# Kernel tuning notes

Hardware: AMD Instinct MI355X
Metric: run time of the kernel (lower is better)

## Reference

```python
import jax, jax.numpy as jnp
import numpy as np

EPS = 1e-5
NUM_HEADS = 16


def layernorm(x, g, b):
    m = jnp.mean(x, axis=-1, keepdims=True)
    v = jnp.mean(jnp.square(x - m), axis=-1, keepdims=True)
    return (x - m) * jax.lax.rsqrt(v + EPS) * g + b


def setup_inputs() -> dict:
    key = jax.random.key(0)
    ks = jax.random.split(key, 8)
    B, S, E, F = 16, 512, 1024, 4096
    s_e = 1.0 / np.sqrt(E)
    s_f = 1.0 / np.sqrt(F)
    return {
        "input": jax.random.normal(ks[0], (B, S, E), jnp.float32),
        "ln1_g": jnp.ones((E,), jnp.float32),
        "ln1_b": jnp.zeros((E,), jnp.float32),
        "wq": jax.random.normal(ks[1], (E, E), jnp.float32) * s_e,
        "bq": jnp.zeros((E,), jnp.float32),
        "wk": jax.random.normal(ks[2], (E, E), jnp.float32) * s_e,
        "bk": jnp.zeros((E,), jnp.float32),
        "wv": jax.random.normal(ks[3], (E, E), jnp.float32) * s_e,
        "bv": jnp.zeros((E,), jnp.float32),
        "wo": jax.random.normal(ks[4], (E, E), jnp.float32) * s_e,
        "bo": jnp.zeros((E,), jnp.float32),
        "ln2_g": jnp.ones((E,), jnp.float32),
        "ln2_b": jnp.zeros((E,), jnp.float32),
        "w1": jax.random.normal(ks[5], (E, F), jnp.float32) * s_e,
        "b1": jnp.zeros((F,), jnp.float32),
        "w2": jax.random.normal(ks[6], (F, E), jnp.float32) * s_f,
        "b2": jnp.zeros((E,), jnp.float32),
    }


def attention(x, wq, bq, wk, bk, wv, bv, wo, bo):
    B, S, E = x.shape
    H = NUM_HEADS
    D = E // H
    q = (x @ wq + bq).reshape(B, S, H, D)
    k = (x @ wk + bk).reshape(B, S, H, D)
    v = (x @ wv + bv).reshape(B, S, H, D)
    scores = jnp.einsum("bqhd,bkhd->bhqk", q, k) * (1.0 / np.sqrt(D))
    attn = jax.nn.softmax(scores, axis=-1)
    out = jnp.einsum("bhqk,bkhd->bqhd", attn, v).reshape(B, S, E)
    return out @ wo + bo


def reference(input, ln1_g, ln1_b, wq, bq, wk, bk, wv, bv, wo, bo,
              ln2_g, ln2_b, w1, b1, w2, b2):
    # pre-LN attention + residual
    x = layernorm(input, ln1_g, ln1_b)
    x = attention(x, wq, bq, wk, bk, wv, bv, wo, bo)
    x = x + input
    # pre-LN MLP (GELU exact, matching nn.GELU default) + residual
    y = layernorm(x, ln2_g, ln2_b)
    y = jax.nn.gelu(y @ w1 + b1, approximate=False)
    y = y @ w2 + b2
    return x + y
```

## Files before the change

### kernel.cpp

```cpp
#include <hip/hip_runtime.h>
#include <hip/hip_bf16.h>


typedef __bf16 bf16x8 __attribute__((ext_vector_type(8)));
typedef __bf16 bf16x4 __attribute__((ext_vector_type(4)));
typedef float  f32x4  __attribute__((ext_vector_type(4)));

#define EPI_QKV  0
#define EPI_RES  1
#define EPI_GELU 2

__device__ __forceinline__ void async_copy16(const void* g, void* l) {
  __builtin_amdgcn_global_load_lds((const __attribute__((address_space(1))) void*)g,
                                   (__attribute__((address_space(3))) void*)l, 16, 0, 0);
}

__global__ __launch_bounds__(256) void prep_weights(
    const float* __restrict__ wq, const float* __restrict__ wk,
    const float* __restrict__ wv, const float* __restrict__ wo,
    const float* __restrict__ w1, const float* __restrict__ w2,
    const float* __restrict__ bq, const float* __restrict__ bk,
    const float* __restrict__ bv,
    __bf16* __restrict__ wqkvT, __bf16* __restrict__ woT,
    __bf16* __restrict__ w1T, __bf16* __restrict__ w2T, float* __restrict__ bqkv) {
  const int bid = blockIdx.x;
  if (bid >= 12288) {
    const int i = (bid - 12288) * 256 + threadIdx.x;
    bqkv[i] = (i < 1024) ? bq[i] : ((i < 2048) ? bk[i - 1024] : bv[i - 2048]);
    return;
  }
  const float* in;
  __bf16* out;
  int K, N, tile;
  if (bid < 4096) {
    const int w = bid >> 10;
    tile = bid & 1023;
    in = (w == 0) ? wq : (w == 1) ? wk : (w == 2) ? wv : wo;
    out = (w == 3) ? woT : (wqkvT + (size_t)w * 1024 * 1024);
    K = 1024; N = 1024;
  } else if (bid < 8192) { tile = bid - 4096; in = w1; out = w1T; K = 1024; N = 4096; }
  else                   { tile = bid - 8192; in = w2; out = w2T; K = 4096; N = 1024; }
  const int ntx = N >> 5;
  const int bx = tile % ntx, by = tile / ntx;
  const int n0 = bx * 32, k0 = by * 32;

  __shared__ float tilebuf[32][33];
  const int tx = threadIdx.x & 31, ty = threadIdx.x >> 5;
#pragma unroll
  for (int i = 0; i < 4; i++)
    tilebuf[ty + i * 8][tx] = in[(size_t)(k0 + ty + i * 8) * N + n0 + tx];
  __syncthreads();
#pragma unroll
  for (int i = 0; i < 4; i++)
    out[(size_t)(n0 + ty + i * 8) * K + k0 + tx] = (__bf16)tilebuf[tx][ty + i * 8];
}

__device__ __forceinline__ float block_sum(float v, float* red) {
#pragma unroll
  for (int off = 32; off; off >>= 1) v += __shfl_down(v, off);
  const int w = threadIdx.x >> 6;
  __syncthreads();
  if ((threadIdx.x & 63) == 0) red[w] = v;
  __syncthreads();
  return red[0] + red[1] + red[2] + red[3];
}

__global__ __launch_bounds__(256) void ln_kernel(const float* __restrict__ x,
                                                 const float* __restrict__ g,
                                                 const float* __restrict__ bta,
                                                 __bf16* __restrict__ out) {
  __shared__ float red[8];
  const int row = blockIdx.x, t = threadIdx.x;
  const float4 v = ((const float4*)(x + (size_t)row * 1024))[t];
  float s = v.x + v.y + v.z + v.w;
  s = block_sum(s, red);
  const float mean = s * (1.0f / 1024.0f);
  const float d0 = v.x - mean, d1 = v.y - mean, d2 = v.z - mean, d3 = v.w - mean;
  float vs = d0 * d0 + d1 * d1 + d2 * d2 + d3 * d3;
  vs = block_sum(vs, red);
  const float rstd = rsqrtf(vs * (1.0f / 1024.0f) + 1e-5f);
  const float4 gg = ((const float4*)g)[t];
  const float4 bb = ((const float4*)bta)[t];
  bf16x4 o;
  o[0] = (__bf16)(d0 * rstd * gg.x + bb.x);
  o[1] = (__bf16)(d1 * rstd * gg.y + bb.y);
  o[2] = (__bf16)(d2 * rstd * gg.z + bb.z);
  o[3] = (__bf16)(d3 * rstd * gg.w + bb.w);
  ((bf16x4*)out)[(size_t)row * 256 + t] = o;
}

template <int EPI>
__global__ __launch_bounds__(256, 2) void gemm_bt(const __bf16* __restrict__ A,
                                                  const __bf16* __restrict__ Bt,
                                                  const float* __restrict__ bias,
                                                  const float* __restrict__ res,
                                                  void* __restrict__ out,
                                                  void* __restrict__ out2,
                                                  int N, int K) {
  __shared__ __bf16 lA[128 * 64];
  __shared__ __bf16 lB[128 * 64];
  const int t = threadIdx.x;
  const int wave = t >> 6, lane = t & 63;
  const int lm = lane & 15, lq = lane >> 4;

  const int Ntiles = gridDim.x;
  const int flat = blockIdx.y * Ntiles + blockIdx.x;
  const int xcd = flat & 7;
  const int local = flat >> 3;
  const int tn = local % Ntiles;
  const int tm = (local / Ntiles) * 8 + xcd;
  const int m0 = tm * 128, n0 = tn * 128;
  const int wm = (wave & 1) * 64, wn = (wave >> 1) * 64;

  f32x4 acc[4][4] = {};

  const int srow = t >> 3, sslot = t & 7;
  const int schunk = sslot ^ (srow & 7);
  const __bf16* aSrc = A + (size_t)(m0 + srow) * K + schunk * 8;
  const __bf16* bSrc = Bt + (size_t)(n0 + srow) * K + schunk * 8;

  for (int k0 = 0; k0 < K; k0 += 64) {
#pragma unroll
    for (int i = 0; i < 4; i++) {
      async_copy16(aSrc + (size_t)(i * 32) * K, lA + i * 2048 + t * 8);
      async_copy16(bSrc + (size_t)(i * 32) * K, lB + i * 2048 + t * 8);
    }
    aSrc += 64; bSrc += 64;
    __syncthreads();
#pragma unroll
    for (int kk = 0; kk < 2; kk++) {
      bf16x8 af[4], bf[4];
      const int slot = (kk * 4 + lq) ^ (lm & 7);
#pragma unroll
      for (int i = 0; i < 4; i++) {
        af[i] = *(const bf16x8*)&lA[(wm + i * 16 + lm) * 64 + slot * 8];
        bf[i] = *(const bf16x8*)&lB[(wn + i * 16 + lm) * 64 + slot * 8];
      }
#pragma unroll
      for (int mi = 0; mi < 4; mi++)
#pragma unroll
        for (int ni = 0; ni < 4; ni++)
          acc[mi][ni] = __builtin_amdgcn_mfma_f32_16x16x32_bf16(af[mi], bf[ni], acc[mi][ni], 0, 0, 0);
    }
    __syncthreads();
  }

#pragma unroll
  for (int mi = 0; mi < 4; mi++) {
    const int gr = m0 + wm + mi * 16 + lq * 4;
#pragma unroll
    for (int ni = 0; ni < 4; ni++) {
      const int gc = n0 + wn + ni * 16 + lm;
      const float bv = bias[gc];
#pragma unroll
      for (int r = 0; r < 4; r++) {
        float v = acc[mi][ni][r] + bv;
        const int row = gr + r;
        if (EPI == EPI_GELU) {
          v = 0.5f * v * (1.0f + erff(v * 0.70710678118654752f));
          ((__bf16*)out)[(size_t)row * N + gc] = (__bf16)v;
        } else if (EPI == EPI_RES) {
          ((float*)out)[(size_t)row * N + gc] = v + res[(size_t)row * N + gc];
        } else {
          if (gc < 2048) {
            ((__bf16*)out)[(size_t)row * 2048 + gc] = (__bf16)v;
          } else {
            const int d = gc & 63, hh = (gc - 2048) >> 6;
            const int bb = row >> 9, ss = row & 511;
            ((__bf16*)out2)[(((size_t)bb * 16 + hh) * 64 + d) * 512 + ss] = (__bf16)v;
          }
        }
      }
    }
  }
}

#define MFMA_QUAD(MI0)                                                         \
  do {                                                                         \
    _Pragma("unroll") for (int kk = 0; kk < 2; ++kk) {                         \
      _Pragma("unroll") for (int ni = 0; ni < 4; ++ni) {                       \
        acc[MI0][ni] = __builtin_amdgcn_mfma_f32_16x16x32_bf16(                \
            af[MI0][kk], bf[ni][kk], acc[MI0][ni], 0, 0, 0);                   \
        acc[(MI0) + 1][ni] = __builtin_amdgcn_mfma_f32_16x16x32_bf16(          \
            af[(MI0) + 1][kk], bf[ni][kk], acc[(MI0) + 1][ni], 0, 0, 0);       \
      }                                                                        \
    }                                                                          \
  } while (0)

#define READ_A8(MI)                                                            \
  _Pragma("unroll") for (int kk = 0; kk < 2; ++kk)                             \
      af[MI][kk] = *(const bf16x8*)&bufA[(wm * 128 + (MI)*16 + lm) * 64 +      \
                                         (((kk * 4 + lq) ^ sw) * 8)];

template <int EPI>
__global__ __launch_bounds__(512, 2) void gemm8_bt(const __bf16* __restrict__ A,
                                                   const __bf16* __restrict__ Bt,
                                                   const float* __restrict__ bias,
                                                   void* __restrict__ out,
                                                   void* __restrict__ out2,
                                                   int N, int K) {
  __shared__ __bf16 lA[2 * 256 * 64];
  __shared__ __bf16 lB[2 * 256 * 64];
  const int t = threadIdx.x;
  const int wave = t >> 6, lane = t & 63;
  const int lm = lane & 15, lq = lane >> 4, sw = lm & 7;
  const int wm = wave >> 2, wn = wave & 3;

  const int Ntiles = gridDim.x;
  const int flat = blockIdx.y * Ntiles + blockIdx.x;
  const int xcd = flat & 7;
  const int local = flat >> 3;
  const int tn = local % Ntiles;
  const int tm = (local / Ntiles) * 8 + xcd;
  const int m0 = tm * 256, n0 = tn * 256;

  const int NT = K >> 6;

  const int srow = t >> 3;
  const int schunk = (t & 7) ^ (srow & 7);
  const __bf16* aBase = A + (size_t)(m0 + srow) * K + schunk * 8;
  const __bf16* bBase = Bt + (size_t)(n0 + srow) * K + schunk * 8;
  __bf16* ldA = lA + t * 8;
  __bf16* ldB = lB + t * 8;

  auto stage = [&](int h) {
    if (h >= 4 * NT) return;
    const int tau = h >> 2, type = h & 3, hf = type & 1;
    const size_t roff = (size_t)(hf * 128) * K + (size_t)tau * 64;
    const int loff = (tau & 1) * 16384 + hf * 8192;
    if (type < 2) {
      async_copy16(aBase + roff, ldA + loff);
      async_copy16(aBase + roff + (size_t)64 * K, ldA + loff + 4096);
    } else {
      async_copy16(bBase + roff, ldB + loff);
      async_copy16(bBase + roff + (size_t)64 * K, ldB + loff + 4096);
    }
  };

  f32x4 acc[8][4] = {};

  for (int h = 0; h < 6; ++h) stage(h);
  asm volatile("s_waitcnt vmcnt(4)" ::: "memory");
  __builtin_amdgcn_s_barrier();

  for (int tt = 0; tt < NT; ++tt) {
    const __bf16* bufA = lA + (tt & 1) * 16384;
    const __bf16* bufB = lB + (tt & 1) * 16384;
    bf16x8 af[8][2], bf[4][2];

#pragma unroll
    for (int ni = 0; ni < 4; ++ni)
#pragma unroll
      for (int kk = 0; kk < 2; ++kk)
        bf[ni][kk] = *(const bf16x8*)&bufB[(wn * 64 + ni * 16 + lm) * 64 +
                                           (((kk * 4 + lq) ^ sw) * 8)];
    READ_A8(0)
    READ_A8(1)
    stage(4 * tt + 6);
    __builtin_amdgcn_s_barrier();
    asm volatile("s_waitcnt lgkmcnt(0)" ::: "memory");
    __builtin_amdgcn_sched_barrier(0);
    __builtin_amdgcn_s_setprio(1);
    MFMA_QUAD(0);
    __builtin_amdgcn_s_setprio(0);
    __builtin_amdgcn_s_barrier();

    READ_A8(2)
    READ_A8(3)
    READ_A8(4)
    READ_A8(5)
    READ_A8(6)
    READ_A8(7)
    stage(4 * tt + 7);
    __builtin_amdgcn_s_barrier();
    asm volatile("s_waitcnt lgkmcnt(0)" ::: "memory");
    __builtin_amdgcn_sched_barrier(0);
    __builtin_amdgcn_s_setprio(1);
    MFMA_QUAD(2);
    __builtin_amdgcn_s_setprio(0);
    __builtin_amdgcn_s_barrier();

    stage(4 * tt + 8);
    __builtin_amdgcn_s_barrier();
    __builtin_amdgcn_s_setprio(1);
    MFMA_QUAD(4);
    __builtin_amdgcn_s_setprio(0);
    __builtin_amdgcn_s_barrier();

    stage(4 * tt + 9);
    __builtin_amdgcn_s_barrier();
    __builtin_amdgcn_s_setprio(1);
    MFMA_QUAD(6);
    __builtin_amdgcn_s_setprio(0);

    if (tt < NT - 1) {
      if (tt == NT - 2) asm volatile("s_waitcnt vmcnt(0)" ::: "memory");
      else              asm volatile("s_waitcnt vmcnt(4)" ::: "memory");
      __builtin_amdgcn_s_barrier();
    }
  }

#pragma unroll
  for (int mi = 0; mi < 8; ++mi) {
    const int gr = m0 + wm * 128 + mi * 16 + lq * 4;
#pragma unroll
    for (int ni = 0; ni < 4; ++ni) {
      const int gc = n0 + wn * 64 + ni * 16 + lm;
      const float bv = bias[gc];
#pragma unroll
      for (int r = 0; r < 4; ++r) {
        float v = acc[mi][ni][r] + bv;
        const int row = gr + r;
        if (EPI == EPI_GELU) {
          v = 0.5f * v * (1.0f + erff(v * 0.70710678118654752f));
          ((__bf16*)out)[(size_t)row * N + gc] = (__bf16)v;
        } else {
          if (gc < 2048) {
            ((__bf16*)out)[(size_t)row * 2048 + gc] = (__bf16)v;
          } else {
            const int d = gc & 63, hh = (gc - 2048) >> 6;
            const int bb = row >> 9, ss = row & 511;
            ((__bf16*)out2)[(((size_t)bb * 16 + hh) * 64 + d) * 512 + ss] = (__bf16)v;
          }
        }
      }
    }
  }
}

__global__ __launch_bounds__(256) void attn_kernel(const __bf16* __restrict__ qk,
                                                   const __bf16* __restrict__ Vt,
                                                   __bf16* __restrict__ outA) {
  __shared__ __bf16 lK[128 * 64];
  __shared__ __bf16 lV[64 * 128];
  __shared__ __bf16 lP[4][16 * 128];
  const int t = threadIdx.x, wave = t >> 6, lane = t & 63;
  const int lm = lane & 15, lq = lane >> 4;
  const int sw = lm & 7;
  const int flat = blockIdx.x;
  const int xcd = flat & 7, local = flat >> 3;
  const int qt = local & 7;
  const int bh = (local >> 3) * 8 + xcd;
  const int h = bh & 15, b = bh >> 4;
  const int q0 = qt * 64 + wave * 16;

  const size_t qrow = (size_t)(b * 512 + q0 + lm) * 2048 + h * 64;
  bf16x8 aq0 = *(const bf16x8*)&qk[qrow + lq * 8];
  bf16x8 aq1 = *(const bf16x8*)&qk[qrow + 32 + lq * 8];

  float mrow[4] = {-3e38f, -3e38f, -3e38f, -3e38f};
  float lrow[4] = {0.f, 0.f, 0.f, 0.f};
  f32x4 o[4] = {};

  const int krow = t >> 3;
  const int kchunk = (t & 7) ^ (krow & 7);
  const __bf16* kSrc = qk + (size_t)(b * 512 + krow) * 2048 + 1024 + h * 64 + kchunk * 8;
  const int vrow = t >> 4;
  const int vchunk = (t & 15) ^ (vrow & 7);
  const __bf16* vSrc = Vt + ((size_t)bh * 64 + vrow) * 512 + vchunk * 8;

  for (int kt = 0; kt < 4; kt++) {
#pragma unroll
    for (int i = 0; i < 4; i++) {
      async_copy16(kSrc + (size_t)(kt * 128 + i * 32) * 2048, lK + i * 2048 + t * 8);
      async_copy16(vSrc + kt * 128 + (size_t)(i * 16) * 512, lV + i * 2048 + t * 8);
    }
    __syncthreads();

    f32x4 s[8];
#pragma unroll
    for (int ni = 0; ni < 8; ni++) {
      bf16x8 bk0 = *(const bf16x8*)&lK[(ni * 16 + lm) * 64 + ((lq ^ sw) * 8)];
      bf16x8 bk1 = *(const bf16x8*)&lK[(ni * 16 + lm) * 64 + (((4 + lq) ^ sw) * 8)];
      f32x4 z = {};
      z = __builtin_amdgcn_mfma_f32_16x16x32_bf16(aq0, bk0, z, 0, 0, 0);
      z = __builtin_amdgcn_mfma_f32_16x16x32_bf16(aq1, bk1, z, 0, 0, 0);
      s[ni] = z;
    }
#pragma unroll
    for (int ni = 0; ni < 8; ni++)
#pragma unroll
      for (int r = 0; r < 4; r++) s[ni][r] *= 0.125f;

    float mnew[4], alpha[4];
#pragma unroll
    for (int r = 0; r < 4; r++) {
      float mx = s[0][r];
#pragma unroll
      for (int ni = 1; ni < 8; ni++) mx = fmaxf(mx, s[ni][r]);
#pragma unroll
      for (int off = 1; off < 16; off <<= 1) mx = fmaxf(mx, __shfl_xor(mx, off));
      mnew[r] = fmaxf(mrow[r], mx);
      alpha[r] = __expf(mrow[r] - mnew[r]);
      mrow[r] = mnew[r];
    }
    float rs[4] = {0.f, 0.f, 0.f, 0.f};
#pragma unroll
    for (int ni = 0; ni < 8; ni++)
#pragma unroll
      for (int r = 0; r < 4; r++) {
        const float p = __expf(s[ni][r] - mnew[r]);
        s[ni][r] = p;
        rs[r] += p;
      }
#pragma unroll
    for (int r = 0; r < 4; r++) {
#pragma unroll
      for (int off = 1; off < 16; off <<= 1) rs[r] += __shfl_xor(rs[r], off);
      lrow[r] = lrow[r] * alpha[r] + rs[r];
    }

#pragma unroll
    for (int ni = 0; ni < 8; ni++) {
      const int chunk = ni * 2 + (lm >> 3);
#pragma unroll
      for (int r = 0; r < 4; r++) {
        const int q = lq * 4 + r;
        lP[wave][q * 128 + ((chunk ^ (q & 7)) * 8) + (lm & 7)] = (__bf16)s[ni][r];
      }
    }
    asm volatile("s_waitcnt lgkmcnt(0)" ::: "memory");
    bf16x8 ap[4];
#pragma unroll
    for (int kc = 0; kc < 4; kc++)
      ap[kc] = *(const bf16x8*)&lP[wave][lm * 128 + (((kc * 4 + lq) ^ sw) * 8)];

#pragma unroll
    for (int di = 0; di < 4; di++)
#pragma unroll
      for (int r = 0; r < 4; r++) o[di][r] *= alpha[r];

#pragma unroll
    for (int di = 0; di < 4; di++) {
#pragma unroll
      for (int kc = 0; kc < 4; kc++) {
        bf16x8 bv = *(const bf16x8*)&lV[(di * 16 + lm) * 128 + (((kc * 4 + lq) ^ sw) * 8)];
        o[di] = __builtin_amdgcn_mfma_f32_16x16x32_bf16(ap[kc], bv, o[di], 0, 0, 0);
      }
    }
    __syncthreads();
  }

#pragma unroll
  for (int di = 0; di < 4; di++)
#pragma unroll
    for (int r = 0; r < 4; r++) {
      const float v = o[di][r] / lrow[r];
      outA[(size_t)(b * 512 + q0 + lq * 4 + r) * 1024 + h * 64 + di * 16 + lm] = (__bf16)v;
    }
}

extern "C" void kernel_launch(void* const* d_in, const int* in_sizes, int n_in,
                              void* d_out, int out_size, void* d_ws, size_t ws_size,
                              hipStream_t stream) {
  const float* input = (const float*)d_in[0];
  const float* ln1_g = (const float*)d_in[1];
  const float* ln1_b = (const float*)d_in[2];
  const float* wq = (const float*)d_in[3];
  const float* bq = (const float*)d_in[4];
  const float* wk = (const float*)d_in[5];
  const float* bk = (const float*)d_in[6];
  const float* wv = (const float*)d_in[7];
  const float* bv = (const float*)d_in[8];
  const float* wo = (const float*)d_in[9];
  const float* bo = (const float*)d_in[10];
  const float* ln2_g = (const float*)d_in[11];
  const float* ln2_b = (const float*)d_in[12];
  const float* w1 = (const float*)d_in[13];
  const float* b1 = (const float*)d_in[14];
  const float* w2 = (const float*)d_in[15];
  const float* b2 = (const float*)d_in[16];

  char* ws = (char*)d_ws;
  __bf16* wqkvT = (__bf16*)(ws + 0);
  __bf16* woT   = (__bf16*)(ws + ((size_t)6 << 20));
  __bf16* w1T   = (__bf16*)(ws + ((size_t)8 << 20));
  __bf16* w2T   = (__bf16*)(ws + ((size_t)16 << 20));
  __bf16* qkbuf = (__bf16*)(ws + ((size_t)24 << 20));
  __bf16* vtbuf = (__bf16*)(ws + ((size_t)56 << 20));
  __bf16* abuf  = (__bf16*)(ws + ((size_t)72 << 20));
  float*  xbuf  = (float*) (ws + ((size_t)24 << 20));
  __bf16* ylnbuf= (__bf16*)(ws + ((size_t)56 << 20));
  __bf16* hbuf  = (__bf16*)(ws + ((size_t)72 << 20));
  float*  bqkv  = (float*) (ws + ((size_t)136 << 20));

  const dim3 blk(256);
  const dim3 blk8(512);
  prep_weights<<<12300, blk, 0, stream>>>(wq, wk, wv, wo, w1, w2, bq, bk, bv,
                                          wqkvT, woT, w1T, w2T, bqkv);

  ln_kernel<<<8192, blk, 0, stream>>>(input, ln1_g, ln1_b, abuf);
  gemm_bt<EPI_QKV><<<dim3(24, 64), blk, 0, stream>>>(abuf, wqkvT, bqkv, nullptr,
                                                     qkbuf, vtbuf, 3072, 1024);
  attn_kernel<<<2048, blk, 0, stream>>>(qkbuf, vtbuf, abuf);
  gemm_bt<EPI_RES><<<dim3(8, 64), blk, 0, stream>>>(abuf, woT, bo, input,
                                                    xbuf, nullptr, 1024, 1024);
  ln_kernel<<<8192, blk, 0, stream>>>(xbuf, ln2_g, ln2_b, ylnbuf);
  gemm8_bt<EPI_GELU><<<dim3(16, 32), blk8, 0, stream>>>(ylnbuf, w1T, b1,
                                                        hbuf, nullptr, 4096, 1024);
  gemm_bt<EPI_RES><<<dim3(8, 64), blk, 0, stream>>>(hbuf, w2T, b2, xbuf,
                                                    d_out, nullptr, 1024, 4096);
}
```

Baseline: 524.5 us.

## Enlarge attention query tile per block and double-buffer K/V loads

Each wave now handles 64 query rows (four 16-row groups) instead of 16, so a block covers 256 queries and the grid shrinks from 2048 to 512 blocks. Each K/V tile staged in shared memory is therefore reused across four times as many queries, cutting global K/V traffic. K/V tiles are double-buffered with async copies and explicit vmcnt waits, so the next tile loads while the current one is computed. The cost is much higher register pressure (16 output accumulators per wave), twice the LDS for K/V, and fewer blocks, which may lower occupancy and leave some CUs idle.

```diff
diff --git a/kernel.cpp b/kernel.cpp
--- a/kernel.cpp
+++ b/kernel.cpp
@@ -328,29 +328,36 @@
   }
 }
 
-__global__ __launch_bounds__(256) void attn_kernel(const __bf16* __restrict__ qk,
-                                                   const __bf16* __restrict__ Vt,
-                                                   __bf16* __restrict__ outA) {
-  __shared__ __bf16 lK[128 * 64];
-  __shared__ __bf16 lV[64 * 128];
+__global__ __launch_bounds__(256, 2) void attn_kernel(const __bf16* __restrict__ qk,
+                                                      const __bf16* __restrict__ Vt,
+                                                      __bf16* __restrict__ outA) {
+  __shared__ __bf16 lK[2][128 * 64];
+  __shared__ __bf16 lV[2][64 * 128];
   __shared__ __bf16 lP[4][16 * 128];
   const int t = threadIdx.x, wave = t >> 6, lane = t & 63;
   const int lm = lane & 15, lq = lane >> 4;
   const int sw = lm & 7;
   const int flat = blockIdx.x;
   const int xcd = flat & 7, local = flat >> 3;
-  const int qt = local & 7;
-  const int bh = (local >> 3) * 8 + xcd;
+  const int qt = local & 1;
+  const int bh = xcd * 32 + (local >> 1);
   const int h = bh & 15, b = bh >> 4;
-  const int q0 = qt * 64 + wave * 16;
-
-  const size_t qrow = (size_t)(b * 512 + q0 + lm) * 2048 + h * 64;
-  bf16x8 aq0 = *(const bf16x8*)&qk[qrow + lq * 8];
-  bf16x8 aq1 = *(const bf16x8*)&qk[qrow + 32 + lq * 8];
-
-  float mrow[4] = {-3e38f, -3e38f, -3e38f, -3e38f};
-  float lrow[4] = {0.f, 0.f, 0.f, 0.f};
-  f32x4 o[4] = {};
+  const int qbase = qt * 256 + wave * 64;
+
+  bf16x8 aq[4][2];
+#pragma unroll
+  for (int qg = 0; qg < 4; qg++) {
+    const size_t qrow = (size_t)(b * 512 + qbase + qg * 16 + lm) * 2048 + h * 64;
+    aq[qg][0] = *(const bf16x8*)&qk[qrow + lq * 8];
+    aq[qg][1] = *(const bf16x8*)&qk[qrow + 32 + lq * 8];
+  }
+
+  float mrow[4][4], lrow[4][4];
+  f32x4 o[4][4] = {};
+#pragma unroll
+  for (int qg = 0; qg < 4; qg++)
+#pragma unroll
+    for (int r = 0; r < 4; r++) { mrow[qg][r] = -3e38f; lrow[qg][r] = 0.f; }
 
   const int krow = t >> 3;
   const int kchunk = (t & 7) ^ (krow & 7);
@@ -359,95 +366,114 @@
   const int vchunk = (t & 15) ^ (vrow & 7);
   const __bf16* vSrc = Vt + ((size_t)bh * 64 + vrow) * 512 + vchunk * 8;
 
+  auto stage = [&](int kt) {
+    __bf16* dK = &lK[kt & 1][t * 8];
+    __bf16* dV = &lV[kt & 1][t * 8];
+#pragma unroll
+    for (int i = 0; i < 4; i++) {
+      async_copy16(kSrc + (size_t)(kt * 128 + i * 32) * 2048, dK + i * 2048);
+      async_copy16(vSrc + kt * 128 + (size_t)(i * 16) * 512, dV + i * 2048);
+    }
+  };
+
+  stage(0);
   for (int kt = 0; kt < 4; kt++) {
-#pragma unroll
-    for (int i = 0; i < 4; i++) {
-      async_copy16(kSrc + (size_t)(kt * 128 + i * 32) * 2048, lK + i * 2048 + t * 8);
-      async_copy16(vSrc + kt * 128 + (size_t)(i * 16) * 512, lV + i * 2048 + t * 8);
-    }
-    __syncthreads();
-
-    f32x4 s[8];
-#pragma unroll
-    for (int ni = 0; ni < 8; ni++) {
-      bf16x8 bk0 = *(const bf16x8*)&lK[(ni * 16 + lm) * 64 + ((lq ^ sw) * 8)];
-      bf16x8 bk1 = *(const bf16x8*)&lK[(ni * 16 + lm) * 64 + (((4 + lq) ^ sw) * 8)];
-      f32x4 z = {};
-      z = __builtin_amdgcn_mfma_f32_16x16x32_bf16(aq0, bk0, z, 0, 0, 0);
-      z = __builtin_amdgcn_mfma_f32_16x16x32_bf16(aq1, bk1, z, 0, 0, 0);
-      s[ni] = z;
-    }
-#pragma unroll
-    for (int ni = 0; ni < 8; ni++)
-#pragma unroll
-      for (int r = 0; r < 4; r++) s[ni][r] *= 0.125f;
-
-    float mnew[4], alpha[4];
-#pragma unroll
-    for (int r = 0; r < 4; r++) {
-      float mx = s[0][r];
-#pragma unroll
-      for (int ni = 1; ni < 8; ni++) mx = fmaxf(mx, s[ni][r]);
-#pragma unroll
-      for (int off = 1; off < 16; off <<= 1) mx = fmaxf(mx, __shfl_xor(mx, off));
-      mnew[r] = fmaxf(mrow[r], mx);
-      alpha[r] = __expf(mrow[r] - mnew[r]);
-      mrow[r] = mnew[r];
-    }
-    float rs[4] = {0.f, 0.f, 0.f, 0.f};
-#pragma unroll
-    for (int ni = 0; ni < 8; ni++)
+    if (kt < 3) {
+      stage(kt + 1);
+      asm volatile("s_waitcnt vmcnt(8)" ::: "memory");
+    } else {
+      asm volatile("s_waitcnt vmcnt(0)" ::: "memory");
+    }
+    __builtin_amdgcn_s_barrier();
+    const __bf16* bK = lK[kt & 1];
+    const __bf16* bV = lV[kt & 1];
+
+#pragma unroll
+    for (int qg = 0; qg < 4; qg++) {
+      f32x4 s[8];
+#pragma unroll
+      for (int ni = 0; ni < 8; ni++) {
+        bf16x8 bk0 = *(const bf16x8*)&bK[(ni * 16 + lm) * 64 + ((lq ^ sw) * 8)];
+        bf16x8 bk1 = *(const bf16x8*)&bK[(ni * 16 + lm) * 64 + (((4 + lq) ^ sw) * 8)];
+        f32x4 z = {};
+        z = __builtin_amdgcn_mfma_f32_16x16x32_bf16(aq[qg][0], bk0, z, 0, 0, 0);
+        z = __builtin_amdgcn_mfma_f32_16x16x32_bf16(aq[qg][1], bk1, z, 0, 0, 0);
+        s[ni] = z;
+      }
+#pragma unroll
+      for (int ni = 0; ni < 8; ni++)
+#pragma unroll
+        for (int r = 0; r < 4; r++) s[ni][r] *= 0.125f;
+
+      float mnew[4], alpha[4];
 #pragma unroll
       for (int r = 0; r < 4; r++) {
-        const float p = __expf(s[ni][r] - mnew[r]);
-        s[ni][r] = p;
-        rs[r] += p;
-      }
-#pragma unroll
-    for (int r = 0; r < 4; r++) {
-#pragma unroll
-      for (int off = 1; off < 16; off <<= 1) rs[r] += __shfl_xor(rs[r], off);
-      lrow[r] = lrow[r] * alpha[r] + rs[r];
-    }
-
-#pragma unroll
-    for (int ni = 0; ni < 8; ni++) {
-      const int chunk = ni * 2 + (lm >> 3);
+        float mx = s[0][r];
+#pragma unroll
+        for (int ni = 1; ni < 8; ni++) mx = fmaxf(mx, s[ni][r]);
+#pragma unroll
+        for (int off = 1; off < 16; off <<= 1) mx = fmaxf(mx, __shfl_xor(mx, off));
+        mnew[r] = fmaxf(mrow[qg][r], mx);
+        alpha[r] = __expf(mrow[qg][r] - mnew[r]);
+        mrow[qg][r] = mnew[r];
+      }
+      float rs[4] = {0.f, 0.f, 0.f, 0.f};
+#pragma unroll
+      for (int ni = 0; ni < 8; ni++)
+#pragma unroll
+        for (int r = 0; r < 4; r++) {
+          const float p = __expf(s[ni][r] - mnew[r]);
+          s[ni][r] = p;
+          rs[r] += p;
+        }
 #pragma unroll
       for (int r = 0; r < 4; r++) {
-        const int q = lq * 4 + r;
-        lP[wave][q * 128 + ((chunk ^ (q & 7)) * 8) + (lm & 7)] = (__bf16)s[ni][r];
-      }
-    }
-    asm volatile("s_waitcnt lgkmcnt(0)" ::: "memory");
-    bf16x8 ap[4];
-#pragma unroll
-    for (int kc = 0; kc < 4; kc++)
-      ap[kc] = *(const bf16x8*)&lP[wave][lm * 128 + (((kc * 4 + lq) ^ sw) * 8)];
-
+#pragma unroll
+        for (int off = 1; off < 16; off <<= 1) rs[r] += __shfl_xor(rs[r], off);
+        lrow[qg][r] = lrow[qg][r] * alpha[r] + rs[r];
+      }
+
+#pragma unroll
+      for (int ni = 0; ni < 8; ni++) {
+        const int chunk = ni * 2 + (lm >> 3);
+#pragma unroll
+        for (int r = 0; r < 4; r++) {
+          const int q = lq * 4 + r;
+          lP[wave][q * 128 + ((chunk ^ (q & 7)) * 8) + (lm & 7)] = (__bf16)s[ni][r];
+        }
+      }
+      asm volatile("s_waitcnt lgkmcnt(0)" ::: "memory");
+      bf16x8 ap[4];
+#pragma unroll
+      for (int kc = 0; kc < 4; kc++)
+        ap[kc] = *(const bf16x8*)&lP[wave][lm * 128 + (((kc * 4 + lq) ^ sw) * 8)];
+
+#pragma unroll
+      for (int di = 0; di < 4; di++)
+#pragma unroll
+        for (int r = 0; r < 4; r++) o[qg][di][r] *= alpha[r];
+
+#pragma unroll
+      for (int di = 0; di < 4; di++) {
+#pragma unroll
+        for (int kc = 0; kc < 4; kc++) {
+          bf16x8 bv = *(const bf16x8*)&bV[(di * 16 + lm) * 128 + (((kc * 4 + lq) ^ sw) * 8)];
+          o[qg][di] = __builtin_amdgcn_mfma_f32_16x16x32_bf16(ap[kc], bv, o[qg][di], 0, 0, 0);
+        }
+      }
+    }
+    __builtin_amdgcn_s_barrier();
+  }
+
+#pragma unroll
+  for (int qg = 0; qg < 4; qg++)
 #pragma unroll
     for (int di = 0; di < 4; di++)
 #pragma unroll
-      for (int r = 0; r < 4; r++) o[di][r] *= alpha[r];
-
-#pragma unroll
-    for (int di = 0; di < 4; di++) {
-#pragma unroll
-      for (int kc = 0; kc < 4; kc++) {
-        bf16x8 bv = *(const bf16x8*)&lV[(di * 16 + lm) * 128 + (((kc * 4 + lq) ^ sw) * 8)];
-        o[di] = __builtin_amdgcn_mfma_f32_16x16x32_bf16(ap[kc], bv, o[di], 0, 0, 0);
-      }
-    }
-    __syncthreads();
-  }
-
-#pragma unroll
-  for (int di = 0; di < 4; di++)
-#pragma unroll
-    for (int r = 0; r < 4; r++) {
-      const float v = o[di][r] / lrow[r];
-      outA[(size_t)(b * 512 + q0 + lq * 4 + r) * 1024 + h * 64 + di * 16 + lm] = (__bf16)v;
-    }
+      for (int r = 0; r < 4; r++) {
+        const float v = o[qg][di][r] / lrow[qg][r];
+        outA[(size_t)(b * 512 + qbase + qg * 16 + lq * 4 + r) * 1024 + h * 64 + di * 16 + lm] = (__bf16)v;
+      }
 }
 
 extern "C" void kernel_launch(void* const* d_in, const int* in_sizes, int n_in,
@@ -492,7 +518,7 @@
   ln_kernel<<<8192, blk, 0, stream>>>(input, ln1_g, ln1_b, abuf);
   gemm_bt<EPI_QKV><<<dim3(24, 64), blk, 0, stream>>>(abuf, wqkvT, bqkv, nullptr,
                                                      qkbuf, vtbuf, 3072, 1024);
-  attn_kernel<<<2048, blk, 0, stream>>>(qkbuf, vtbuf, abuf);
+  attn_kernel<<<512, blk, 0, stream>>>(qkbuf, vtbuf, abuf);
   gemm_bt<EPI_RES><<<dim3(8, 64), blk, 0, stream>>>(abuf, woT, bo, input,
                                                     xbuf, nullptr, 1024, 1024);
   ln_kernel<<<8192, blk, 0, stream>>>(xbuf, ln2_g, ln2_b, ylnbuf);
```

New measurement: 551.5 us, median of 2. 1.05x slower.
